# Optimization experiments

Hardware: AMD Instinct MI355X
Metric: run time of the kernel (lower is better)

Reference implementation:

```python
import jax, jax.numpy as jnp
import numpy as np

N = 200000
E = 600000
H = 128
NUM_EDGE_TYPES = 16
LN_EPS = 1e-5


def setup_inputs() -> dict:
    key = jax.random.key(0)
    ks = jax.random.split(key, 10)
    x = jax.random.normal(ks[0], (N, H), dtype=jnp.float32)
    edge_index = jax.random.randint(ks[1], (2, E), 0, N, dtype=jnp.int32)
    edge_types = jax.random.randint(ks[2], (E,), 0, NUM_EDGE_TYPES, dtype=jnp.int32)
    s = 1.0 / np.sqrt(H)
    edge_emb = jax.random.normal(ks[3], (NUM_EDGE_TYPES, H), dtype=jnp.float32)
    W_self = jax.random.uniform(ks[4], (H, H), dtype=jnp.float32, minval=-s, maxval=s)
    b_self = jax.random.uniform(ks[5], (H,), dtype=jnp.float32, minval=-s, maxval=s)
    W_msg = jax.random.uniform(ks[6], (H, H), dtype=jnp.float32, minval=-s, maxval=s)
    b_msg = jax.random.uniform(ks[7], (H,), dtype=jnp.float32, minval=-s, maxval=s)
    gamma = jnp.ones((H,), dtype=jnp.float32)
    beta = jnp.zeros((H,), dtype=jnp.float32)
    return {
        "x": x, "edge_index": edge_index, "edge_types": edge_types,
        "edge_emb": edge_emb, "W_self": W_self, "b_self": b_self,
        "W_msg": W_msg, "b_msg": b_msg, "gamma": gamma, "beta": beta,
    }


def reference(x, edge_index, edge_types, edge_emb, W_self, b_self, W_msg, b_msg, gamma, beta):
    src = edge_index[0]
    dst = edge_index[1]
    # gather source node features + typed edge embedding: [E, H]
    typed_messages = x[src] + edge_emb[edge_types]
    # scatter-add into destination nodes: [N, H]
    aggregated = jnp.zeros_like(x).at[dst].add(typed_messages)
    # linear epilogue (torch Linear: y = x @ W.T + b)
    out = (x @ W_self.T + b_self) + (aggregated @ W_msg.T + b_msg)
    out = jax.nn.relu(out)
    # LayerNorm over last dim
    mu = jnp.mean(out, axis=-1, keepdims=True)
    var = jnp.mean(jnp.square(out - mu), axis=-1, keepdims=True)
    out = (out - mu) * jax.lax.rsqrt(var + LN_EPS) * gamma + beta
    # dropout is identity in eval mode
    return out
```

## Files before the change

kernel.cpp:

```cpp
#include <hip/hip_runtime.h>
#include <stdint.h>

#define H 128
#define TM 16
#define MAXDEG 24
#define BSTRIDE 32
#define BSTR16 16
#define OVFCAP 4096

typedef __attribute__((ext_vector_type(8))) short short8;
typedef __attribute__((ext_vector_type(4))) float f32x4;
typedef __attribute__((ext_vector_type(4))) int i32x4;

__device__ __forceinline__ unsigned short f2bf(float f) {
    union { float f; unsigned u; } v; v.f = f;
    unsigned u = v.u;
    u += 0x7fffu + ((u >> 16) & 1u);
    return (unsigned short)(u >> 16);
}

__device__ __forceinline__ float bf2f(unsigned short u) {
    union { unsigned u; float f; } v; v.u = ((unsigned)u) << 16; return v.f;
}

__device__ __forceinline__ short8 cvt8(f32x4 a, f32x4 b) {
    short8 r;
    r[0] = (short)f2bf(a.x); r[1] = (short)f2bf(a.y);
    r[2] = (short)f2bf(a.z); r[3] = (short)f2bf(a.w);
    r[4] = (short)f2bf(b.x); r[5] = (short)f2bf(b.y);
    r[6] = (short)f2bf(b.z); r[7] = (short)f2bf(b.w);
    return r;
}

__device__ __forceinline__ void gadd(int entry, const unsigned short* xb,
                                     const short* emb_s, int l, float* acc) {
    int s = entry & 0x3FFFF, t = entry >> 18;
    short8 xv = *(const short8*)(xb + (size_t)s * H + l * 8);
    short8 ev = *(const short8*)&emb_s[t * 136 + l * 8];
#pragma unroll
    for (int j = 0; j < 8; ++j)
        acc[j] += bf2f((unsigned short)xv[j]) + bf2f((unsigned short)ev[j]);
}

__global__ __launch_bounds__(256) void prep_kernel(
    const float* __restrict__ x, const float* __restrict__ emb,
    unsigned short* __restrict__ xb, unsigned short* __restrict__ embb,
    const int* __restrict__ ei, const int* __restrict__ et,
    int* __restrict__ bucket, int* __restrict__ ovf,
    int total8x, int total8, int E, int eb)
{
    const int tid = threadIdx.x;
    const int base = blockIdx.x << 10;
#pragma unroll
    for (int k = 0; k < 4; ++k) {
        int idx = base + (k << 8) + tid;
        if (idx < total8x) {
            f32x4 a = __builtin_nontemporal_load(((const f32x4*)x) + 2 * idx);
            f32x4 b = __builtin_nontemporal_load(((const f32x4*)x) + 2 * idx + 1);
            ((short8*)xb)[idx] = cvt8(a, b);
        } else if (idx < total8) {
            int j = idx - total8x;
            f32x4 a = __builtin_nontemporal_load(((const f32x4*)emb) + 2 * j);
            f32x4 b = __builtin_nontemporal_load(((const f32x4*)emb) + 2 * j + 1);
            ((short8*)embb)[j] = cvt8(a, b);
        }
    }
    int e0 = blockIdx.x * eb;
    int e1 = e0 + eb; if (e1 > E) e1 = E;
    for (int e = e0 + tid; e < e1; e += 256) {
        int src = ei[e];
        int dst = ei[E + e];
        int t   = et[e];
        int entry = src | (t << 18);
        int* row = bucket + ((size_t)dst << 4);
        int pos = atomicAdd(row, 1);
        if (pos < 15) {
            row[1 + pos] = entry;
        } else {
            int j = atomicAdd(ovf, 1);
            if (j < OVFCAP) { ovf[8 + 2 * j] = dst; ovf[8 + 2 * j + 1] = entry; }
        }
    }
}

__global__ __launch_bounds__(256) void prep_edges_kernel(
    const int* __restrict__ ei, const int* __restrict__ et,
    int* __restrict__ cnt, int* __restrict__ bucket, int E)
{
    int e = blockIdx.x * 256 + threadIdx.x;
    if (e >= E) return;
    int src = ei[e];
    int dst = ei[E + e];
    int t   = et[e];
    int pos = atomicAdd(&cnt[dst], 1);
    if (pos < MAXDEG) bucket[(size_t)dst * MAXDEG + pos] = src | (t << 18);
}

__global__ __launch_bounds__(256) void aggregate_bf16_kernel(
    const unsigned short* __restrict__ xb, const unsigned short* __restrict__ embb,
    const int* __restrict__ bucket, const int* __restrict__ ovf,
    const int* __restrict__ ei, const int* __restrict__ et,
    unsigned short* __restrict__ aggb, int N, int E, int T)
{
    __shared__ __align__(16) short emb_s[16 * 136];

    const int tid = threadIdx.x;
    const int l   = tid & 15;
    if (tid < T * 16) {
        int t = tid >> 4;
        *(short8*)&emb_s[t * 136 + l * 8] = *(const short8*)(embb + t * H + l * 8);
    }
    __syncthreads();

    const int nGroups = N >> 4;
    for (int g = blockIdx.x; g < nGroups; g += gridDim.x) {
        const int node = (g << 4) + (tid >> 4);

        const int* row = bucket + ((size_t)node << 4);
        i32x4 q = *(const i32x4*)row;
        const int c = q.x;

        float acc[8] = {0.f, 0.f, 0.f, 0.f, 0.f, 0.f, 0.f, 0.f};

        bool fullscan = false;
        int cc = c, nov = 0;
        if (c > 15) {
            nov = ovf[0];
            if (nov > OVFCAP) fullscan = true;
            cc = 15;
        }

        if (!fullscan) {
            {
                const bool b0 = cc > 0, b1 = cc > 1, b2 = cc > 2;
                short8 xv0, xv1, xv2, ev0, ev1, ev2;
                if (b0) {
                    int s = q.y & 0x3FFFF, t = q.y >> 18;
                    xv0 = *(const short8*)(xb + (size_t)s * H + l * 8);
                    ev0 = *(const short8*)&emb_s[t * 136 + l * 8];
                }
                if (b1) {
                    int s = q.z & 0x3FFFF, t = q.z >> 18;
                    xv1 = *(const short8*)(xb + (size_t)s * H + l * 8);
                    ev1 = *(const short8*)&emb_s[t * 136 + l * 8];
                }
                if (b2) {
                    int s = q.w & 0x3FFFF, t = q.w >> 18;
                    xv2 = *(const short8*)(xb + (size_t)s * H + l * 8);
                    ev2 = *(const short8*)&emb_s[t * 136 + l * 8];
                }
                if (b0) {
#pragma unroll
                    for (int j = 0; j < 8; ++j) acc[j] += bf2f((unsigned short)xv0[j]) + bf2f((unsigned short)ev0[j]);
                }
                if (b1) {
#pragma unroll
                    for (int j = 0; j < 8; ++j) acc[j] += bf2f((unsigned short)xv1[j]) + bf2f((unsigned short)ev1[j]);
                }
                if (b2) {
#pragma unroll
                    for (int j = 0; j < 8; ++j) acc[j] += bf2f((unsigned short)xv2[j]) + bf2f((unsigned short)ev2[j]);
                }
            }
            for (int i0 = 3; i0 < cc; i0 += 4) {
                i32x4 p = *(const i32x4*)(row + 1 + i0);
                const int rem = cc - i0;
                const bool h1 = rem > 1, h2 = rem > 2, h3 = rem > 3;
                short8 xv0, xv1, xv2, xv3, ev0, ev1, ev2, ev3;
                {
                    int s = p.x & 0x3FFFF, t = p.x >> 18;
                    xv0 = *(const short8*)(xb + (size_t)s * H + l * 8);
                    ev0 = *(const short8*)&emb_s[t * 136 + l * 8];
                }
                if (h1) {
                    int s = p.y & 0x3FFFF, t = p.y >> 18;
                    xv1 = *(const short8*)(xb + (size_t)s * H + l * 8);
                    ev1 = *(const short8*)&emb_s[t * 136 + l * 8];
                }
                if (h2) {
                    int s = p.z & 0x3FFFF, t = p.z >> 18;
                    xv2 = *(const short8*)(xb + (size_t)s * H + l * 8);
                    ev2 = *(const short8*)&emb_s[t * 136 + l * 8];
                }
                if (h3) {
                    int s = p.w & 0x3FFFF, t = p.w >> 18;
                    xv3 = *(const short8*)(xb + (size_t)s * H + l * 8);
                    ev3 = *(const short8*)&emb_s[t * 136 + l * 8];
                }
#pragma unroll
                for (int j = 0; j < 8; ++j) acc[j] += bf2f((unsigned short)xv0[j]) + bf2f((unsigned short)ev0[j]);
                if (h1) {
#pragma unroll
                    for (int j = 0; j < 8; ++j) acc[j] += bf2f((unsigned short)xv1[j]) + bf2f((unsigned short)ev1[j]);
                }
                if (h2) {
#pragma unroll
                    for (int j = 0; j < 8; ++j) acc[j] += bf2f((unsigned short)xv2[j]) + bf2f((unsigned short)ev2[j]);
                }
                if (h3) {
#pragma unroll
                    for (int j = 0; j < 8; ++j) acc[j] += bf2f((unsigned short)xv3[j]) + bf2f((unsigned short)ev3[j]);
                }
            }
            if (c > 15) {
                for (int j = 0; j < nov; ++j) {
                    if (ovf[8 + 2 * j] == node) gadd(ovf[8 + 2 * j + 1], xb, emb_s, l, acc);
                }
            }
        } else {
            for (int e = 0; e < E; ++e) {
                if (ei[E + e] == node) gadd(ei[e] | (et[e] << 18), xb, emb_s, l, acc);
            }
        }

        short8 r;
#pragma unroll
        for (int j = 0; j < 8; ++j) r[j] = (short)f2bf(acc[j]);
        *(short8*)(aggb + (size_t)node * H + l * 8) = r;
    }
}

__global__ __launch_bounds__(256) void gemm_ln32_kernel(
    const unsigned short* __restrict__ xb, const unsigned short* __restrict__ aggb,
    const float* __restrict__ Wself, const float* __restrict__ bself,
    const float* __restrict__ Wmsg, const float* __restrict__ bmsg,
    const float* __restrict__ gamma, const float* __restrict__ beta,
    float* __restrict__ out, int nSuper)
{
    __shared__ __align__(16) char smem_u[32 * 264 * 2];
    short* a_stage = (short*)smem_u;
    float* o_stage = (float*)smem_u;

    const int tid  = threadIdx.x;
    const int wave = tid >> 6;
    const int lane = tid & 63;
    const int col  = lane & 15;
    const int quad = lane >> 4;

    short8 bfrag[2][8];
    float bias[2];
#pragma unroll
    for (int s = 0; s < 2; ++s) {
        const int h = (wave * 2 + s) * 16 + col;
        bias[s] = bself[h] + bmsg[h];
#pragma unroll
        for (int kst = 0; kst < 8; ++kst) {
            const float* W = (kst < 4) ? Wself : Wmsg;
            const int k0 = (kst & 3) * 32 + quad * 8;
            const float* p = W + (size_t)h * H + k0;
            bfrag[s][kst] = cvt8(*(const f32x4*)p, *(const f32x4*)(p + 4));
        }
    }

    const int lrow = tid >> 4;
    const int l4 = (tid & 15) * 4;
    f32x4 g0  = *(const f32x4*)(gamma + l4);
    f32x4 g1  = *(const f32x4*)(gamma + 64 + l4);
    f32x4 be0 = *(const f32x4*)(beta + l4);
    f32x4 be1 = *(const f32x4*)(beta + 64 + l4);

    const int srow = tid >> 3;
    const int sq   = tid & 7;

    for (int st = blockIdx.x; st < nSuper; st += gridDim.x) {
        const size_t rowBase = (size_t)st * 32;
        __syncthreads();

        {
            const unsigned short* src = (sq < 4)
                ? (xb   + (rowBase + srow) * H + sq * 32)
                : (aggb + (rowBase + srow) * H + (sq - 4) * 32);
            short* dstl = &a_stage[srow * 264 + (sq & 3) * 32 + ((sq >> 2) << 7)];
            *(short8*)(dstl)      = ((const short8*)src)[0];
            *(short8*)(dstl + 8)  = ((const short8*)src)[1];
            *(short8*)(dstl + 16) = ((const short8*)src)[2];
            *(short8*)(dstl + 24) = ((const short8*)src)[3];
        }
        __syncthreads();

        f32x4 acc00 = {0.f,0.f,0.f,0.f}, acc01 = {0.f,0.f,0.f,0.f};
        f32x4 acc10 = {0.f,0.f,0.f,0.f}, acc11 = {0.f,0.f,0.f,0.f};
        {
            short8 afr[8];
#pragma unroll
            for (int kst = 0; kst < 8; ++kst)
                afr[kst] = *(const short8*)&a_stage[col * 264 + kst * 32 + quad * 8];
#pragma unroll
            for (int kst = 0; kst < 8; ++kst) {
                acc00 = __builtin_amdgcn_mfma_f32_16x16x32_bf16(afr[kst], bfrag[0][kst], acc00, 0, 0, 0);
                acc01 = __builtin_amdgcn_mfma_f32_16x16x32_bf16(afr[kst], bfrag[1][kst], acc01, 0, 0, 0);
            }
#pragma unroll
            for (int kst = 0; kst < 8; ++kst)
                afr[kst] = *(const short8*)&a_stage[(16 + col) * 264 + kst * 32 + quad * 8];
#pragma unroll
            for (int kst = 0; kst < 8; ++kst) {
                acc10 = __builtin_amdgcn_mfma_f32_16x16x32_bf16(afr[kst], bfrag[0][kst], acc10, 0, 0, 0);
                acc11 = __builtin_amdgcn_mfma_f32_16x16x32_bf16(afr[kst], bfrag[1][kst], acc11, 0, 0, 0);
            }
        }
        __syncthreads();

        {
            const int h0 = (wave * 2) * 16 + col;
            const int h1 = h0 + 16;
#pragma unroll
            for (int r = 0; r < 4; ++r) {
                const int m = quad * 4 + r;
                float v;
                v = acc00[r] + bias[0]; o_stage[m * 132 + h0]        = v > 0.f ? v : 0.f;
                v = acc01[r] + bias[1]; o_stage[m * 132 + h1]        = v > 0.f ? v : 0.f;
                v = acc10[r] + bias[0]; o_stage[(16 + m) * 132 + h0] = v > 0.f ? v : 0.f;
                v = acc11[r] + bias[1]; o_stage[(16 + m) * 132 + h1] = v > 0.f ? v : 0.f;
            }
        }
        __syncthreads();

#pragma unroll
        for (int half = 0; half < 2; ++half) {
            const int row = half * 16 + lrow;
            const float* orow = &o_stage[row * 132];
            f32x4 va = *(const f32x4*)(orow + l4);
            f32x4 vb = *(const f32x4*)(orow + 64 + l4);

            float s1 = (va.x + va.y + va.z + va.w) + (vb.x + vb.y + vb.z + vb.w);
            float s2 = va.x*va.x + va.y*va.y + va.z*va.z + va.w*va.w
                     + vb.x*vb.x + vb.y*vb.y + vb.z*vb.z + vb.w*vb.w;
#pragma unroll
            for (int m = 1; m < 16; m <<= 1) {
                s1 += __shfl_xor(s1, m, 64);
                s2 += __shfl_xor(s2, m, 64);
            }
            const float mu = s1 * (1.f / 128.f);
            const float var = s2 * (1.f / 128.f) - mu * mu;
            const float rstd = rsqrtf(var + 1e-5f);

            f32x4 o0, o1;
            o0.x = (va.x - mu) * rstd * g0.x + be0.x;
            o0.y = (va.y - mu) * rstd * g0.y + be0.y;
            o0.z = (va.z - mu) * rstd * g0.z + be0.z;
            o0.w = (va.w - mu) * rstd * g0.w + be0.w;
            o1.x = (vb.x - mu) * rstd * g1.x + be1.x;
            o1.y = (vb.y - mu) * rstd * g1.y + be1.y;
            o1.z = (vb.z - mu) * rstd * g1.z + be1.z;
            o1.w = (vb.w - mu) * rstd * g1.w + be1.w;

            float* dst = out + (rowBase + row) * H;
            __builtin_nontemporal_store(o0, (f32x4*)(dst + l4));
            __builtin_nontemporal_store(o1, (f32x4*)(dst + 64 + l4));
        }
    }
}

__global__ __launch_bounds__(256) void aggregate_f32_kernel(
    const float* __restrict__ x, const float* __restrict__ emb,
    const int* __restrict__ cnt, const int* __restrict__ bucket,
    const int* __restrict__ ei, const int* __restrict__ et,
    unsigned short* __restrict__ aggb, int N, int E, int T)
{
    __shared__ __align__(16) float emb_s[16 * 132];

    const int tid = threadIdx.x;
    for (int i = tid; i < T * H; i += 256)
        emb_s[(i >> 7) * 132 + (i & 127)] = emb[i];
    __syncthreads();

    const int l = tid & 15;
    const int nGroups = N >> 4;

    for (int g = blockIdx.x; g < nGroups; g += gridDim.x) {
        const int node = (g << 4) + (tid >> 4);
        const int* b = bucket + (size_t)node * MAXDEG;
        i32x4 p = *(const i32x4*)b;
        const int c = cnt[node];

        f32x4 acc0 = {0.f,0.f,0.f,0.f};
        f32x4 acc1 = {0.f,0.f,0.f,0.f};

        if (c <= MAXDEG) {
            for (int i0 = 0; i0 < c; i0 += 4) {
                if (i0 > 0) p = *(const i32x4*)(b + i0);
                const int rem = c - i0;
                const bool h1 = rem > 1, h2 = rem > 2, h3 = rem > 3;
                f32x4 x00,x01,e00,e01,x10,x11,e10,e11,x20,x21,e20,e21,x30,x31,e30,e31;
                {
                    int s = p.x & 0x3FFFF, t = p.x >> 18;
                    const float* xp = x + (size_t)s * H + l * 8;
                    const float* ep = emb_s + t * 132 + l * 8;
                    x00 = *(const f32x4*)xp; x01 = *(const f32x4*)(xp + 4);
                    e00 = *(const f32x4*)ep; e01 = *(const f32x4*)(ep + 4);
                }
                if (h1) {
                    int s = p.y & 0x3FFFF, t = p.y >> 18;
                    const float* xp = x + (size_t)s * H + l * 8;
                    const float* ep = emb_s + t * 132 + l * 8;
                    x10 = *(const f32x4*)xp; x11 = *(const f32x4*)(xp + 4);
                    e10 = *(const f32x4*)ep; e11 = *(const f32x4*)(ep + 4);
                }
                if (h2) {
                    int s = p.z & 0x3FFFF, t = p.z >> 18;
                    const float* xp = x + (size_t)s * H + l * 8;
                    const float* ep = emb_s + t * 132 + l * 8;
                    x20 = *(const f32x4*)xp; x21 = *(const f32x4*)(xp + 4);
                    e20 = *(const f32x4*)ep; e21 = *(const f32x4*)(ep + 4);
                }
                if (h3) {
                    int s = p.w & 0x3FFFF, t = p.w >> 18;
                    const float* xp = x + (size_t)s * H + l * 8;
                    const float* ep = emb_s + t * 132 + l * 8;
                    x30 = *(const f32x4*)xp; x31 = *(const f32x4*)(xp + 4);
                    e30 = *(const f32x4*)ep; e31 = *(const f32x4*)(ep + 4);
                }
                acc0 += x00 + e00;  acc1 += x01 + e01;
                if (h1) { acc0 += x10 + e10;  acc1 += x11 + e11; }
                if (h2) { acc0 += x20 + e20;  acc1 += x21 + e21; }
                if (h3) { acc0 += x30 + e30;  acc1 += x31 + e31; }
            }
        } else {
            for (int e = 0; e < E; ++e) {
                if (ei[E + e] == node) {
                    int s = ei[e], t = et[e];
                    const float* xp = x + (size_t)s * H + l * 8;
                    const float* ep = emb_s + t * 132 + l * 8;
                    f32x4 a0 = *(const f32x4*)xp, a1 = *(const f32x4*)(xp + 4);
                    f32x4 b0 = *(const f32x4*)ep, b1 = *(const f32x4*)(ep + 4);
                    acc0 += a0 + b0;  acc1 += a1 + b1;
                }
            }
        }
        *(short8*)(aggb + (size_t)node * H + l * 8) = cvt8(acc0, acc1);
    }
}

__global__ __launch_bounds__(256) void gemm_ln16_kernel(
    const float* __restrict__ x, const unsigned short* __restrict__ aggb,
    const float* __restrict__ Wself, const float* __restrict__ bself,
    const float* __restrict__ Wmsg, const float* __restrict__ bmsg,
    const float* __restrict__ gamma, const float* __restrict__ beta,
    float* __restrict__ out, int nTiles)
{
    __shared__ __align__(16) short a_stage[TM * 264];
    __shared__ __align__(16) float o_stage[TM * 132];

    const int tid  = threadIdx.x;
    const int wave = tid >> 6;
    const int lane = tid & 63;
    const int col  = lane & 15;
    const int quad = lane >> 4;

    short8 bfrag[2][8];
    float bias[2];
#pragma unroll
    for (int s = 0; s < 2; ++s) {
        const int h = (wave * 2 + s) * 16 + col;
        bias[s] = bself[h] + bmsg[h];
#pragma unroll
        for (int kst = 0; kst < 8; ++kst) {
            const float* W = (kst < 4) ? Wself : Wmsg;
            const int k0 = (kst & 3) * 32 + quad * 8;
            const float* p = W + (size_t)h * H + k0;
            bfrag[s][kst] = cvt8(*(const f32x4*)p, *(const f32x4*)(p + 4));
        }
    }

    const int lnode = tid >> 4;
    const int f0 = (tid & 15) * 8;
    f32x4 g0  = *(const f32x4*)(gamma + f0);
    f32x4 g1  = *(const f32x4*)(gamma + f0 + 4);
    f32x4 be0 = *(const f32x4*)(beta + f0);
    f32x4 be1 = *(const f32x4*)(beta + f0 + 4);

    const int node = tid >> 4;
    const int seg  = tid & 15;

    for (int tile = blockIdx.x; tile < nTiles; tile += gridDim.x) {
        const size_t rowBase = (size_t)tile * TM;
        if (seg < 8) {
            const float* src = x + (rowBase + node) * H + seg * 16;
            f32x4 v0 = ((const f32x4*)src)[0];
            f32x4 v1 = ((const f32x4*)src)[1];
            f32x4 v2 = ((const f32x4*)src)[2];
            f32x4 v3 = ((const f32x4*)src)[3];
            *(short8*)&a_stage[node * 264 + seg * 16]     = cvt8(v0, v1);
            *(short8*)&a_stage[node * 264 + seg * 16 + 8] = cvt8(v2, v3);
        } else {
            const unsigned short* src = aggb + (rowBase + node) * H + (seg - 8) * 16;
            *(short8*)&a_stage[node * 264 + 128 + (seg - 8) * 16]     = *(const short8*)src;
            *(short8*)&a_stage[node * 264 + 128 + (seg - 8) * 16 + 8] = *(const short8*)(src + 8);
        }
        __syncthreads();

        short8 afr[8];
#pragma unroll
        for (int kst = 0; kst < 8; ++kst)
            afr[kst] = *(const short8*)(&a_stage[col * 264 + kst * 32 + quad * 8]);

        f32x4 acc0 = {0.f,0.f,0.f,0.f};
        f32x4 acc1 = {0.f,0.f,0.f,0.f};
#pragma unroll
        for (int kst = 0; kst < 8; ++kst) {
            acc0 = __builtin_amdgcn_mfma_f32_16x16x32_bf16(afr[kst], bfrag[0][kst], acc0, 0, 0, 0);
            acc1 = __builtin_amdgcn_mfma_f32_16x16x32_bf16(afr[kst], bfrag[1][kst], acc1, 0, 0, 0);
        }

#pragma unroll
        for (int s = 0; s < 2; ++s) {
            const int h = (wave * 2 + s) * 16 + col;
            f32x4 a = s ? acc1 : acc0;
#pragma unroll
            for (int r = 0; r < 4; ++r) {
                const int m = quad * 4 + r;
                float v = a[r] + bias[s];
                o_stage[m * 132 + h] = v > 0.f ? v : 0.f;
            }
        }
        __syncthreads();

        float v[8];
        float s1 = 0.f, s2 = 0.f;
#pragma unroll
        for (int j = 0; j < 8; ++j) {
            v[j] = o_stage[lnode * 132 + f0 + j];
            s1 += v[j];
            s2 += v[j] * v[j];
        }
#pragma unroll
        for (int m = 1; m < 16; m <<= 1) {
            s1 += __shfl_xor(s1, m, 64);
            s2 += __shfl_xor(s2, m, 64);
        }
        const float mu = s1 * (1.f / 128.f);
        const float var = s2 * (1.f / 128.f) - mu * mu;
        const float rstd = rsqrtf(var + 1e-5f);

        f32x4 o0, o1;
        o0.x = (v[0] - mu) * rstd * g0.x + be0.x;
        o0.y = (v[1] - mu) * rstd * g0.y + be0.y;
        o0.z = (v[2] - mu) * rstd * g0.z + be0.z;
        o0.w = (v[3] - mu) * rstd * g0.w + be0.w;
        o1.x = (v[4] - mu) * rstd * g1.x + be1.x;
        o1.y = (v[5] - mu) * rstd * g1.y + be1.y;
        o1.z = (v[6] - mu) * rstd * g1.z + be1.z;
        o1.w = (v[7] - mu) * rstd * g1.w + be1.w;

        float* dst = out + (rowBase + lnode) * H + f0;
        __builtin_nontemporal_store(o0, (f32x4*)dst);
        __builtin_nontemporal_store(o1, (f32x4*)(dst + 4));
    }
}

__global__ __launch_bounds__(256) void scatter_kernel(
    const float* __restrict__ x, const int* __restrict__ ei,
    const int* __restrict__ et, const float* __restrict__ emb,
    float* __restrict__ agg, int E)
{
    int g = blockIdx.x * 256 + threadIdx.x;
    int e = g >> 5;
    int l = g & 31;
    if (e >= E) return;
    int src = ei[e];
    int dst = ei[E + e];
    int t   = et[e];
    f32x4 xv = *(const f32x4*)(x   + (size_t)src * H + l * 4);
    f32x4 ev = *(const f32x4*)(emb + (size_t)t   * H + l * 4);
    float* b = agg + (size_t)dst * H + l * 4;
    atomicAdd(b + 0, xv.x + ev.x);
    atomicAdd(b + 1, xv.y + ev.y);
    atomicAdd(b + 2, xv.z + ev.z);
    atomicAdd(b + 3, xv.w + ev.w);
}

__global__ __launch_bounds__(256) void gemm_ln_f32_kernel(
    const float* __restrict__ x,
    const float* __restrict__ Wself, const float* __restrict__ bself,
    const float* __restrict__ Wmsg, const float* __restrict__ bmsg,
    const float* __restrict__ gamma, const float* __restrict__ beta,
    float* __restrict__ out, int nTiles)
{
    __shared__ __align__(16) short a_stage[TM * 264];
    __shared__ __align__(16) float o_stage[TM * 132];

    const int tid  = threadIdx.x;
    const int wave = tid >> 6;
    const int lane = tid & 63;
    const int col  = lane & 15;
    const int quad = lane >> 4;

    short8 bfrag[2][8];
    float bias[2];
#pragma unroll
    for (int s = 0; s < 2; ++s) {
        const int h = (wave * 2 + s) * 16 + col;
        bias[s] = bself[h] + bmsg[h];
#pragma unroll
        for (int kst = 0; kst < 8; ++kst) {
            const float* W = (kst < 4) ? Wself : Wmsg;
            const int k0 = (kst & 3) * 32 + quad * 8;
            const float* p = W + (size_t)h * H + k0;
            bfrag[s][kst] = cvt8(*(const f32x4*)p, *(const f32x4*)(p + 4));
        }
    }

    const int lnode = tid >> 4;
    const int f0 = (tid & 15) * 8;
    f32x4 g0  = *(const f32x4*)(gamma + f0);
    f32x4 g1  = *(const f32x4*)(gamma + f0 + 4);
    f32x4 be0 = *(const f32x4*)(beta + f0);
    f32x4 be1 = *(const f32x4*)(beta + f0 + 4);

    for (int tile = blockIdx.x; tile < nTiles; tile += gridDim.x) {
        const size_t rowBase = (size_t)tile * TM;
        {
            const int node = tid >> 4;
            const int seg  = tid & 15;
            const int k0   = seg * 16;
            const float* src = (seg < 8)
                ? (x   + (rowBase + node) * H + k0)
                : (out + (rowBase + node) * H + (k0 - 128));
            f32x4 v0 = ((const f32x4*)src)[0];
            f32x4 v1 = ((const f32x4*)src)[1];
            f32x4 v2 = ((const f32x4*)src)[2];
            f32x4 v3 = ((const f32x4*)src)[3];
            *(short8*)(&a_stage[node * 264 + k0])     = cvt8(v0, v1);
            *(short8*)(&a_stage[node * 264 + k0 + 8]) = cvt8(v2, v3);
        }
        __syncthreads();

        short8 afr[8];
#pragma unroll
        for (int kst = 0; kst < 8; ++kst)
            afr[kst] = *(const short8*)(&a_stage[col * 264 + kst * 32 + quad * 8]);

        f32x4 acc0 = {0.f,0.f,0.f,0.f};
        f32x4 acc1 = {0.f,0.f,0.f,0.f};
#pragma unroll
        for (int kst = 0; kst < 8; ++kst) {
            acc0 = __builtin_amdgcn_mfma_f32_16x16x32_bf16(afr[kst], bfrag[0][kst], acc0, 0, 0, 0);
            acc1 = __builtin_amdgcn_mfma_f32_16x16x32_bf16(afr[kst], bfrag[1][kst], acc1, 0, 0, 0);
        }

#pragma unroll
        for (int s = 0; s < 2; ++s) {
            const int h = (wave * 2 + s) * 16 + col;
            f32x4 a = s ? acc1 : acc0;
#pragma unroll
            for (int r = 0; r < 4; ++r) {
                const int m = quad * 4 + r;
                float v = a[r] + bias[s];
                o_stage[m * 132 + h] = v > 0.f ? v : 0.f;
            }
        }
        __syncthreads();

        float v[8];
        float s1 = 0.f, s2 = 0.f;
#pragma unroll
        for (int j = 0; j < 8; ++j) {
            v[j] = o_stage[lnode * 132 + f0 + j];
            s1 += v[j];
            s2 += v[j] * v[j];
        }
#pragma unroll
        for (int m = 1; m < 16; m <<= 1) {
            s1 += __shfl_xor(s1, m, 64);
            s2 += __shfl_xor(s2, m, 64);
        }
        const float mu = s1 * (1.f / 128.f);
        const float var = s2 * (1.f / 128.f) - mu * mu;
        const float rstd = rsqrtf(var + 1e-5f);

        f32x4 o0, o1;
        o0.x = (v[0] - mu) * rstd * g0.x + be0.x;
        o0.y = (v[1] - mu) * rstd * g0.y + be0.y;
        o0.z = (v[2] - mu) * rstd * g0.z + be0.z;
        o0.w = (v[3] - mu) * rstd * g0.w + be0.w;
        o1.x = (v[4] - mu) * rstd * g1.x + be1.x;
        o1.y = (v[5] - mu) * rstd * g1.y + be1.y;
        o1.z = (v[6] - mu) * rstd * g1.z + be1.z;
        o1.w = (v[7] - mu) * rstd * g1.w + be1.w;

        float* dst = out + (rowBase + lnode) * H + f0;
        *(f32x4*)(dst)     = o0;
        *(f32x4*)(dst + 4) = o1;
    }
}

extern "C" void kernel_launch(void* const* d_in, const int* in_sizes, int n_in,
                              void* d_out, int out_size, void* d_ws, size_t ws_size,
                              hipStream_t stream) {
    const float* x     = (const float*)d_in[0];
    const int*   ei    = (const int*)d_in[1];
    const int*   et    = (const int*)d_in[2];
    const float* emb   = (const float*)d_in[3];
    const float* Wself = (const float*)d_in[4];
    const float* bself = (const float*)d_in[5];
    const float* Wmsg  = (const float*)d_in[6];
    const float* bmsg  = (const float*)d_in[7];
    const float* gamma = (const float*)d_in[8];
    const float* beta  = (const float*)d_in[9];
    float* out = (float*)d_out;

    const int E = in_sizes[2];
    const int N = in_sizes[0] / H;
    const int T = in_sizes[3] / H;
    const int nTiles = N / TM;

    auto rnd = [](size_t b) { return (b + 255) & ~(size_t)255; };
    const size_t sz_xb    = rnd((size_t)N * H * 2);
    const size_t sz_embb  = rnd((size_t)T * H * 2);
    const size_t sz_agg   = rnd((size_t)N * H * 2);
    const size_t sz_bkt16 = rnd((size_t)N * BSTR16 * 4);
    const size_t sz_ovf   = rnd((size_t)(8 + 2 * OVFCAP) * 4);
    const size_t sz_cnt   = rnd((size_t)N * 4);
    const size_t sz_bkt24 = rnd((size_t)N * MAXDEG * 4);
    const size_t needA = sz_xb + sz_embb + sz_agg + sz_bkt16 + sz_ovf;
    const size_t needB = sz_agg + sz_cnt + sz_bkt24;

    const bool okT = (T <= 16) && (N <= (1 << 18));
    const bool tierA = okT && (ws_size >= needA) && (N % 32 == 0);
    const bool tierB = okT && (ws_size >= needB) && (N % TM == 0);

    if (tierA) {
        uint8_t* p = (uint8_t*)d_ws;
        unsigned short* xb   = (unsigned short*)p;  p += sz_xb;
        unsigned short* embb = (unsigned short*)p;  p += sz_embb;
        unsigned short* aggb = (unsigned short*)p;  p += sz_agg;
        int* bucket = (int*)p;                      p += sz_bkt16;
        int* ovf    = (int*)p;

        hipMemsetAsync(bucket, 0, sz_bkt16 + sz_ovf, stream);

        const int t8x = N * H / 8, t8e = T * H / 8;
        const int total8 = t8x + t8e;
        const int nConv = (total8 + 1023) >> 10;
        const int eb = (E + nConv - 1) / nConv;
        prep_kernel<<<nConv, 256, 0, stream>>>(
            x, emb, xb, embb, ei, et, bucket, ovf, t8x, total8, E, eb);

        const int nGroups = N >> 4;
        int aggGrid = nGroups < 6250 ? nGroups : 6250;
        aggregate_bf16_kernel<<<aggGrid, 256, 0, stream>>>(
            xb, embb, bucket, ovf, ei, et, aggb, N, E, T);

        const int nSuper = N / 32;
        int gemmGrid = nSuper < 8192 ? nSuper : 8192;
        gemm_ln32_kernel<<<gemmGrid, 256, 0, stream>>>(
            xb, aggb, Wself, bself, Wmsg, bmsg, gamma, beta, out, nSuper);
    } else if (tierB) {
        uint8_t* p = (uint8_t*)d_ws;
        unsigned short* aggb = (unsigned short*)p;  p += sz_agg;
        int* cnt    = (int*)p;                      p += sz_cnt;
        int* bucket = (int*)p;

        hipMemsetAsync(cnt, 0, (size_t)N * sizeof(int), stream);

        if (E > 0) {
            prep_edges_kernel<<<(E + 255) / 256, 256, 0, stream>>>(
                ei, et, cnt, bucket, E);
        }
        const int nGroups = N >> 4;
        int aggGrid = nGroups < 4096 ? nGroups : 4096;
        aggregate_f32_kernel<<<aggGrid, 256, 0, stream>>>(
            x, emb, cnt, bucket, ei, et, aggb, N, E, T);

        int gemmGrid = nTiles < 2048 ? nTiles : 2048;
        gemm_ln16_kernel<<<gemmGrid, 256, 0, stream>>>(
            x, aggb, Wself, bself, Wmsg, bmsg, gamma, beta, out, nTiles);
    } else {
        hipMemsetAsync(out, 0, (size_t)N * H * sizeof(float), stream);
        const long long sthreads = (long long)E * 32;
        scatter_kernel<<<(int)((sthreads + 255) / 256), 256, 0, stream>>>(
            x, ei, et, emb, out, E);
        int grid = 2500;
        if (grid > nTiles) grid = nTiles;
        gemm_ln_f32_kernel<<<grid, 256, 0, stream>>>(
            x, Wself, bself, Wmsg, bmsg, gamma, beta, out, nTiles);
    }
}
```

Before: 353.8 us.

## Prefetch next GEMM tile into registers and flatten prep kernel indexing

The persistent GEMM+LayerNorm kernel now loads the next 32-row tile of xb/aggb into registers while the current tile is computed. It splits the shared staging buffer into separate A and output regions so one barrier can be dropped, and caps the grid at 3125 blocks so each block handles several tiles. The prep kernel is changed to one element per thread, covering both the conversion and the edge bucketing with a flat index instead of per-block chunking. The cost is more registers and LDS per block, which may reduce occupancy.

```diff
diff --git a/kernel.cpp b/kernel.cpp
--- a/kernel.cpp
+++ b/kernel.cpp
@@ -4,7 +4,6 @@
 #define H 128
 #define TM 16
 #define MAXDEG 24
-#define BSTRIDE 32
 #define BSTR16 16
 #define OVFCAP 4096
 
@@ -47,30 +46,23 @@
     unsigned short* __restrict__ xb, unsigned short* __restrict__ embb,
     const int* __restrict__ ei, const int* __restrict__ et,
     int* __restrict__ bucket, int* __restrict__ ovf,
-    int total8x, int total8, int E, int eb)
+    int total8x, int total8e, int E)
 {
-    const int tid = threadIdx.x;
-    const int base = blockIdx.x << 10;
-#pragma unroll
-    for (int k = 0; k < 4; ++k) {
-        int idx = base + (k << 8) + tid;
-        if (idx < total8x) {
-            f32x4 a = __builtin_nontemporal_load(((const f32x4*)x) + 2 * idx);
-            f32x4 b = __builtin_nontemporal_load(((const f32x4*)x) + 2 * idx + 1);
-            ((short8*)xb)[idx] = cvt8(a, b);
-        } else if (idx < total8) {
-            int j = idx - total8x;
-            f32x4 a = __builtin_nontemporal_load(((const f32x4*)emb) + 2 * j);
-            f32x4 b = __builtin_nontemporal_load(((const f32x4*)emb) + 2 * j + 1);
-            ((short8*)embb)[j] = cvt8(a, b);
-        }
-    }
-    int e0 = blockIdx.x * eb;
-    int e1 = e0 + eb; if (e1 > E) e1 = E;
-    for (int e = e0 + tid; e < e1; e += 256) {
-        int src = ei[e];
-        int dst = ei[E + e];
-        int t   = et[e];
+    int i = blockIdx.x * 256 + threadIdx.x;
+    if (i < total8x) {
+        f32x4 a = __builtin_nontemporal_load(((const f32x4*)x) + 2 * i);
+        f32x4 b = __builtin_nontemporal_load(((const f32x4*)x) + 2 * i + 1);
+        ((short8*)xb)[i] = cvt8(a, b);
+    } else if (i < total8x + total8e) {
+        int j = i - total8x;
+        f32x4 a = __builtin_nontemporal_load(((const f32x4*)emb) + 2 * j);
+        f32x4 b = __builtin_nontemporal_load(((const f32x4*)emb) + 2 * j + 1);
+        ((short8*)embb)[j] = cvt8(a, b);
+    }
+    if (i < E) {
+        int src = ei[i];
+        int dst = ei[E + i];
+        int t   = et[i];
         int entry = src | (t << 18);
         int* row = bucket + ((size_t)dst << 4);
         int pos = atomicAdd(row, 1);
@@ -227,9 +219,8 @@
     const float* __restrict__ gamma, const float* __restrict__ beta,
     float* __restrict__ out, int nSuper)
 {
-    __shared__ __align__(16) char smem_u[32 * 264 * 2];
-    short* a_stage = (short*)smem_u;
-    float* o_stage = (float*)smem_u;
+    __shared__ __align__(16) short a_stage[32 * 264];
+    __shared__ __align__(16) float o_stage[32 * 132];
 
     const int tid  = threadIdx.x;
     const int wave = tid >> 6;
@@ -261,20 +252,37 @@
 
     const int srow = tid >> 3;
     const int sq   = tid & 7;
-
-    for (int st = blockIdx.x; st < nSuper; st += gridDim.x) {
+    const size_t soff = (sq < 4)
+        ? ((size_t)srow * H + sq * 32)
+        : ((size_t)srow * H + (sq - 4) * 32);
+    const unsigned short* sbase0 = (sq < 4) ? xb : aggb;
+    short* dstl = &a_stage[srow * 264 + (sq & 3) * 32 + ((sq >> 2) << 7)];
+
+    short8 r0, r1, r2, r3;
+    int st = blockIdx.x;
+    if (st < nSuper) {
+        const unsigned short* s = sbase0 + (size_t)st * 32 * H + soff;
+        r0 = ((const short8*)s)[0];
+        r1 = ((const short8*)s)[1];
+        r2 = ((const short8*)s)[2];
+        r3 = ((const short8*)s)[3];
+    }
+
+    for (; st < nSuper; st += gridDim.x) {
         const size_t rowBase = (size_t)st * 32;
-        __syncthreads();
-
-        {
-            const unsigned short* src = (sq < 4)
-                ? (xb   + (rowBase + srow) * H + sq * 32)
-                : (aggb + (rowBase + srow) * H + (sq - 4) * 32);
-            short* dstl = &a_stage[srow * 264 + (sq & 3) * 32 + ((sq >> 2) << 7)];
-            *(short8*)(dstl)      = ((const short8*)src)[0];
-            *(short8*)(dstl + 8)  = ((const short8*)src)[1];
-            *(short8*)(dstl + 16) = ((const short8*)src)[2];
-            *(short8*)(dstl + 24) = ((const short8*)src)[3];
+
+        *(short8*)(dstl)      = r0;
+        *(short8*)(dstl + 8)  = r1;
+        *(short8*)(dstl + 16) = r2;
+        *(short8*)(dstl + 24) = r3;
+
+        const int stn = st + gridDim.x;
+        if (stn < nSuper) {
+            const unsigned short* s = sbase0 + (size_t)stn * 32 * H + soff;
+            r0 = ((const short8*)s)[0];
+            r1 = ((const short8*)s)[1];
+            r2 = ((const short8*)s)[2];
+            r3 = ((const short8*)s)[3];
         }
         __syncthreads();
 
@@ -299,7 +307,6 @@
                 acc11 = __builtin_amdgcn_mfma_f32_16x16x32_bf16(afr[kst], bfrag[1][kst], acc11, 0, 0, 0);
             }
         }
-        __syncthreads();
 
         {
             const int h0 = (wave * 2) * 16 + col;
@@ -731,11 +738,9 @@
         hipMemsetAsync(bucket, 0, sz_bkt16 + sz_ovf, stream);
 
         const int t8x = N * H / 8, t8e = T * H / 8;
-        const int total8 = t8x + t8e;
-        const int nConv = (total8 + 1023) >> 10;
-        const int eb = (E + nConv - 1) / nConv;
-        prep_kernel<<<nConv, 256, 0, stream>>>(
-            x, emb, xb, embb, ei, et, bucket, ovf, t8x, total8, E, eb);
+        int prepWork = (t8x + t8e) > E ? (t8x + t8e) : E;
+        prep_kernel<<<(prepWork + 255) / 256, 256, 0, stream>>>(
+            x, emb, xb, embb, ei, et, bucket, ovf, t8x, t8e, E);
 
         const int nGroups = N >> 4;
         int aggGrid = nGroups < 6250 ? nGroups : 6250;
@@ -743,7 +748,7 @@
             xb, embb, bucket, ovf, ei, et, aggb, N, E, T);
 
         const int nSuper = N / 32;
-        int gemmGrid = nSuper < 8192 ? nSuper : 8192;
+        int gemmGrid = nSuper < 3125 ? nSuper : 3125;
         gemm_ln32_kernel<<<gemmGrid, 256, 0, stream>>>(
             xb, aggb, Wself, bself, Wmsg, bmsg, gamma, beta, out, nSuper);
     } else if (tierB) {
```

Measured after the change: 318.2 us. 1.11x faster.
